# Optimization experiments

Measured on AMD Instinct MI355X. Metric: run time of the kernel, lower is better.

The kernel has to match this reference:

```python
import jax, jax.numpy as jnp
import numpy as np

B, S, D_IN, H, D_OUT = 32, 2048, 256, 512, 256


def setup_inputs() -> dict:
    key = jax.random.key(0)
    ks = jax.random.split(key, 12)
    sc = 0.02
    return {
        "x": jax.random.normal(ks[0], (B, S, D_IN), dtype=jnp.float32),
        # layer 0 (input_dim -> 4H), weights stored (in, out) so y = x @ W + b
        "Wx0": jax.random.normal(ks[1], (D_IN, 4 * H), dtype=jnp.float32) * sc,
        "bx0": jnp.zeros((4 * H,), dtype=jnp.float32),
        "Wh0": jax.random.normal(ks[2], (H, 4 * H), dtype=jnp.float32) * sc,
        "bh0": jnp.zeros((4 * H,), dtype=jnp.float32),
        # layer 1 (hidden -> 4H)
        "Wx1": jax.random.normal(ks[3], (H, 4 * H), dtype=jnp.float32) * sc,
        "bx1": jnp.zeros((4 * H,), dtype=jnp.float32),
        "Wh1": jax.random.normal(ks[4], (H, 4 * H), dtype=jnp.float32) * sc,
        "bh1": jnp.zeros((4 * H,), dtype=jnp.float32),
        # output projection
        "Wfc": jax.random.normal(ks[5], (H, D_OUT), dtype=jnp.float32) * sc,
        "bfc": jnp.zeros((D_OUT,), dtype=jnp.float32),
    }


def _cell(inp, h, c, Wx, bx, Wh, bh):
    # gates chunked in order f, i, g, o (matches torch chunk(4, dim=1))
    gates = inp @ Wx + bx + h @ Wh + bh  # [B, 4H]
    f, i, g, o = jnp.split(gates, 4, axis=1)
    c_new = jax.nn.sigmoid(f) * c + jax.nn.sigmoid(i) * jnp.tanh(g)
    h_new = jax.nn.sigmoid(o) * jnp.tanh(c_new)
    return h_new, c_new


def reference(x, Wx0, bx0, Wh0, bh0, Wx1, bx1, Wh1, bh1, Wfc, bfc):
    b = x.shape[0]
    hdim = Wh0.shape[0]

    def step(carry, xt):
        h0, c0, h1, c1 = carry
        h0, c0 = _cell(xt, h0, c0, Wx0, bx0, Wh0, bh0)
        h1, c1 = _cell(h0, h1, c1, Wx1, bx1, Wh1, bh1)
        return (h0, c0, h1, c1), h1

    init = tuple(jnp.zeros((b, hdim), x.dtype) for _ in range(4))
    x_tfirst = jnp.swapaxes(x, 0, 1)  # [S, B, D_in]
    _, outs = jax.lax.scan(step, init, x_tfirst)  # [S, B, H]
    outs = jnp.swapaxes(outs, 0, 1)  # [B, S, H]
    return outs @ Wfc + bfc  # [B, S, D_out]
```

## Files before the change

kernel.cpp:

```cpp
#include <hip/hip_runtime.h>
#include <math.h>

#define B_    32
#define S_    2048
#define DIN   256
#define H_    512
#define G_    2048
#define DOUT  256
#define T_    2048
#define NBLK  200

typedef __attribute__((ext_vector_type(8))) _Float16 f16x8;
typedef __attribute__((ext_vector_type(16))) float f32x16;
typedef __attribute__((ext_vector_type(2))) float f32x2;

#define MFMA(a,b,c) __builtin_amdgcn_mfma_f32_32x32x16_f16((a),(b),(c),0,0,0)

#define OB_SLOT      0u
#define OB_H0H       16384u
#define OB_H1H       147456u
#define OB_PART      278528u
#define OB_STATE_END 1327104u
#define OB_B0        1327104u
#define OB_B1        1335296u
#define OB_WF        1343488u
#define OB_W0        1605632u
#define OB_W1        4751360u
#define OB_END       8945664u
#define OB_XH        8945664u
#define OB_XEND      42500096u

#define LS_PT    49152
#define LS_CST   65536
#define LS_TOTAL 66560

__device__ __forceinline__ float sigf(float v) {
    return 1.0f / (1.0f + exp2f(-1.44269504f * v));
}
__device__ __forceinline__ float tanhfast(float v) {
    const float e = exp2f(2.88539008f * v);
    return 1.0f - 2.0f / (e + 1.0f);
}
__device__ __forceinline__ unsigned short h2u(_Float16 h) {
    union { _Float16 h; unsigned short u; } v; v.h = h; return v.u;
}

__device__ __forceinline__ f16x8 ld128_coh(const unsigned short* p) {
    f16x8 r;
    asm volatile("global_load_dwordx4 %0, %1, off sc0 sc1"
                 : "=v"(r) : "v"(p) : "memory");
    return r;
}
__device__ __forceinline__ f32x2 ld64f_coh(const float* p) {
    f32x2 r;
    asm volatile("global_load_dwordx2 %0, %1, off sc0 sc1"
                 : "=v"(r) : "v"(p) : "memory");
    return r;
}
__device__ __forceinline__ void st64f_coh(float* p, f32x2 v) {
    asm volatile("global_store_dwordx2 %0, %1, off sc0 sc1"
                 :: "v"(p), "v"(v) : "memory");
}
__device__ __forceinline__ int ld_slot(const int* slots, int i) {
    return __hip_atomic_load(&slots[i * 16], __ATOMIC_RELAXED, __HIP_MEMORY_SCOPE_AGENT);
}
__device__ __forceinline__ int packcol(int p) {
    return (((p >> 2) & 3) * H_) + ((p >> 4) << 2) + (p & 3);
}

__global__ __launch_bounds__(256) void repack_w(
    const float* __restrict__ s1, const float* __restrict__ s2,
    int k1, int K, int srcld, int dopack, unsigned short* __restrict__ dst)
{
    const int p  = blockIdx.x;
    const int kk = blockIdx.y * 256 + threadIdx.x;
    if (kk >= K) return;
    const int oc = dopack ? packcol(p) : p;
    const float w = (kk < k1) ? s1[(size_t)kk * srcld + oc]
                              : s2[(size_t)(kk - k1) * srcld + oc];
    dst[(size_t)p * K + kk] = h2u((_Float16)w);
}

__global__ __launch_bounds__(256) void repack_bias(
    const float* __restrict__ bx0, const float* __restrict__ bh0,
    const float* __restrict__ bx1, const float* __restrict__ bh1,
    char* __restrict__ wsb)
{
    const int q = blockIdx.x * 256 + threadIdx.x;
    if (q >= 2 * G_) return;
    const int p  = q & (G_ - 1);
    const int oc = packcol(p);
    float* dst = (float*)(wsb + (q < G_ ? OB_B0 : OB_B1));
    dst[p] = (q < G_) ? (bx0[oc] + bh0[oc]) : (bx1[oc] + bh1[oc]);
}

__global__ __launch_bounds__(256) void repack_x(const float* __restrict__ x, char* __restrict__ wsb)
{
    unsigned short* xh = (unsigned short*)(wsb + OB_XH);
    const size_t n = (size_t)B_ * S_ * DIN;
    for (size_t i = (size_t)blockIdx.x * 256 + threadIdx.x; i < n; i += (size_t)gridDim.x * 256)
        xh[i] = h2u((_Float16)x[i]);
}

__device__ __forceinline__ void phase_mm_l0(
    int k0, int colc, int halfl, int t, int xsplit,
    const float* __restrict__ x, const unsigned short* __restrict__ XH,
    const unsigned short* A1, const unsigned short* Wlds, f32x16& acc)
{
    f16x8 fh[6];
    #pragma unroll
    for (int s = 0; s < 6; ++s) {
        const int kf = k0 + s * 16;
        if (kf < 256) {
            const size_t o = ((size_t)colc * S_ + t) * DIN + kf + halfl * 8;
            if (xsplit) {
                fh[s] = *(const f16x8*)(XH + o);
            } else {
                const float* xp = x + o;
                #pragma unroll
                for (int j = 0; j < 8; ++j) fh[s][j] = (_Float16)xp[j];
            }
        } else {
            fh[s] = ld128_coh(A1 + colc * 512 + (kf - 256) + halfl * 8);
        }
    }
    asm volatile("s_waitcnt vmcnt(0)" ::: "memory");
    __builtin_amdgcn_sched_barrier(0);
    #pragma unroll
    for (int s = 0; s < 6; ++s) {
        const int k8a = ((k0 + s * 16) >> 3) + halfl;
        const f16x8 bw = *(const f16x8*)(Wlds + (k8a * 32 + colc) * 8);
        acc = MFMA(fh[s], bw, acc);
    }
}

__device__ __forceinline__ void phase_mm_single(
    int k0, int colc, int halfl,
    const unsigned short* A, const unsigned short* Wlds, f32x16& acc)
{
    f16x8 fh[4];
    #pragma unroll
    for (int s = 0; s < 4; ++s)
        fh[s] = ld128_coh(A + colc * 512 + (k0 + s * 16) + halfl * 8);
    asm volatile("s_waitcnt vmcnt(0)" ::: "memory");
    __builtin_amdgcn_sched_barrier(0);
    #pragma unroll
    for (int s = 0; s < 4; ++s) {
        const int k8a = ((k0 + s * 16) >> 3) + halfl;
        const f16x8 bw = *(const f16x8*)(Wlds + (k8a * 32 + colc) * 8);
        acc = MFMA(fh[s], bw, acc);
    }
}

__global__ __launch_bounds__(512, 2) void lstm_persist(
    const float* __restrict__ x, const float* __restrict__ bfc,
    float* __restrict__ out, char* __restrict__ wsb, int xsplit)
{
    extern __shared__ char smem[];
    unsigned short* Wlds = (unsigned short*)smem;
    float* Pt   = (float*)(smem + LS_PT);
    float* cstL = (float*)(smem + LS_CST);
    int* slots  = (int*)(wsb + OB_SLOT);

    const int blk = blockIdx.x, tid = threadIdx.x;
    const int wave = tid >> 6, lane = tid & 63;
    const int colc = lane & 31, halfl = lane >> 5;

    int role, bb;
    if (blk < 64)       { role = 0; bb = blk; }
    else if (blk < 128) { role = 1; bb = blk - 64; }
    else if (blk < 192) { role = 2; bb = blk - 128; }
    else                { role = 3; bb = blk - 192; }

    const int p0 = bb * 32;

    {
        const unsigned short* Wg;
        int wstride, rowoff, kcnt;
        if (role == 0)      { Wg = (const unsigned short*)(wsb + OB_W0); wstride = 768;  rowoff = 0;   kcnt = 768; }
        else if (role == 1) { Wg = (const unsigned short*)(wsb + OB_W1); wstride = 1024; rowoff = 0;   kcnt = 512; }
        else if (role == 2) { Wg = (const unsigned short*)(wsb + OB_W1); wstride = 1024; rowoff = 512; kcnt = 512; }
        else                { Wg = (const unsigned short*)(wsb + OB_WF); wstride = 512;  rowoff = 0;   kcnt = 512; }
        for (int idx = tid; idx < (kcnt >> 3) * 32; idx += 512) {
            const int k8 = idx >> 5, cl = idx & 31;
            *(f16x8*)(Wlds + idx * 8) =
                *(const f16x8*)(Wg + ((size_t)(p0 + cl) * wstride + rowoff + k8 * 8));
        }
    }
    for (int i = tid; i < 256; i += 512) cstL[i] = 0.f;
    __syncthreads();

    unsigned short* H0H = (unsigned short*)(wsb + OB_H0H);
    unsigned short* H1H = (unsigned short*)(wsb + OB_H1H);
    float* PART = (float*)(wsb + OB_PART);
    const unsigned short* XH = (const unsigned short*)(wsb + OB_XH);
    const float* Bp = (const float*)(wsb + (role == 2 ? OB_B1 : OB_B0));

    const int kcnt = (role == 0) ? 768 : 512;
    const int k0 = wave * (kcnt >> 3);
    int sA = 0, sB = 0, sC = 0;

    for (int t = 0; t < T_; ++t) {
        if (tid < 64) {
            if (role == 0) {
                const int tA = t, tB = t - 3;
                for (;;) {
                    bool ok = true;
                    if (sA < tA) sA = ld_slot(slots, lane);
                    ok = ok && (sA >= tA);
                    if (sB < tB) sB = ld_slot(slots, 64 + lane);
                    ok = ok && (sB >= tB);
                    if (__all(ok)) break;
                    __builtin_amdgcn_s_sleep(1);
                }
            } else if (role == 1) {
                const int tA = t + 1, tB = t - 3;
                for (;;) {
                    bool ok = true;
                    if (sA < tA) sA = ld_slot(slots, lane);
                    ok = ok && (sA >= tA);
                    if (lane == 0) {
                        if (sB < tB) sB = ld_slot(slots, 128 + bb);
                        ok = ok && (sB >= tB);
                    }
                    if (__all(ok)) break;
                    __builtin_amdgcn_s_sleep(1);
                }
            } else if (role == 2) {
                const int tA = t, tB = t + 1, tC = t - 3;
                for (;;) {
                    bool ok = true;
                    if (sA < tA) sA = ld_slot(slots, 128 + lane);
                    ok = ok && (sA >= tA);
                    if (lane == 0) {
                        if (sB < tB) sB = ld_slot(slots, 64 + bb);
                        ok = ok && (sB >= tB);
                    }
                    if (lane < 8) {
                        if (sC < tC) sC = ld_slot(slots, 192 + lane);
                        ok = ok && (sC >= tC);
                    }
                    if (__all(ok)) break;
                    __builtin_amdgcn_s_sleep(1);
                }
            } else {
                const int tA = t + 1;
                for (;;) {
                    if (sA < tA) sA = ld_slot(slots, 128 + lane);
                    if (__all(sA >= tA)) break;
                    __builtin_amdgcn_s_sleep(1);
                }
            }
        }
        __syncthreads();

        const int pw = t & 3, pr = (t + 3) & 3;

        f32x2 preg = {0.f, 0.f};
        if (role == 2)
            preg = ld64f_coh(PART + ((size_t)(pw * 64 + bb) << 10) + tid * 2);

        f32x16 acc;
        #pragma unroll
        for (int i = 0; i < 16; ++i) acc[i] = 0.f;

        if (role == 0)
            phase_mm_l0(k0, colc, halfl, t, xsplit, x, XH, H0H + pr * 16384, Wlds, acc);
        else if (role == 1)
            phase_mm_single(k0, colc, halfl, H0H + pw * 16384, Wlds, acc);
        else if (role == 2)
            phase_mm_single(k0, colc, halfl, H1H + pr * 16384, Wlds, acc);
        else
            phase_mm_single(k0, colc, halfl, H1H + pw * 16384, Wlds, acc);

        if (wave >= 4) {
            #pragma unroll
            for (int rg = 0; rg < 16; ++rg) {
                const int row = (rg & 3) + 8 * (rg >> 2) + 4 * halfl;
                Pt[(wave - 4) * 1024 + row * 32 + colc] = acc[rg];
            }
        }
        __syncthreads();
        if (wave < 4) {
            #pragma unroll
            for (int rg = 0; rg < 16; ++rg) {
                const int row = (rg & 3) + 8 * (rg >> 2) + 4 * halfl;
                Pt[wave * 1024 + row * 32 + colc] += acc[rg];
            }
        }
        __syncthreads();

        if (role == 1) {
            f32x2 pv;
            #pragma unroll
            for (int ii = 0; ii < 2; ++ii) {
                const int idx = tid * 2 + ii;
                pv[ii] = Pt[idx] + Pt[1024 + idx] + Pt[2048 + idx] + Pt[3072 + idx];
            }
            st64f_coh(PART + ((size_t)(pw * 64 + bb) << 10) + tid * 2, pv);
        } else if (role == 3) {
            #pragma unroll
            for (int ii = 0; ii < 2; ++ii) {
                const int idx = tid * 2 + ii;
                const int r = idx >> 5, c = idx & 31;
                const float v = Pt[idx] + Pt[1024 + idx] + Pt[2048 + idx] + Pt[3072 + idx]
                              + bfc[p0 + c];
                out[((size_t)r * S_ + t) * DOUT + p0 + c] = v;
            }
        } else {
            #pragma unroll
            for (int ii = 0; ii < 2; ++ii) {
                const int idx = tid * 2 + ii;
                float v = Pt[idx] + Pt[1024 + idx] + Pt[2048 + idx] + Pt[3072 + idx]
                        + Bp[p0 + (idx & 31)];
                if (role == 2) v += preg[ii];
                Pt[idx] = v;
            }
            __syncthreads();
            if (tid < 128) {
                const int r = tid >> 2, u2 = (tid & 3) * 2;
                const int cb = ((u2 >> 2) << 4) + (u2 & 3);
                unsigned short uh[2];
                #pragma unroll
                for (int uu = 0; uu < 2; ++uu) {
                    const float fg = Pt[r * 32 + cb + uu + 0];
                    const float ig = Pt[r * 32 + cb + uu + 4];
                    const float gg = Pt[r * 32 + cb + uu + 8];
                    const float og = Pt[r * 32 + cb + uu + 12];
                    const float cv = cstL[r * 8 + u2 + uu];
                    const float cn = sigf(fg) * cv + sigf(ig) * tanhfast(gg);
                    const float hn = sigf(og) * tanhfast(cn);
                    cstL[r * 8 + u2 + uu] = cn;
                    uh[uu] = h2u((_Float16)hn);
                }
                const unsigned wv = (unsigned)uh[0] | ((unsigned)uh[1] << 16);
                const int off = pw * 16384 + r * 512 + bb * 8 + u2;
                unsigned short* DH = (role == 0) ? H0H : H1H;
                __hip_atomic_store((unsigned*)(DH + off), wv,
                                   __ATOMIC_RELAXED, __HIP_MEMORY_SCOPE_AGENT);
            }
        }

        __syncthreads();
        if (tid == 0)
            __hip_atomic_store(&slots[blk * 16], t + 1,
                               __ATOMIC_RELAXED, __HIP_MEMORY_SCOPE_AGENT);
    }
}

extern "C" void kernel_launch(void* const* d_in, const int* in_sizes, int n_in,
                              void* d_out, int out_size, void* d_ws, size_t ws_size,
                              hipStream_t stream)
{
    const float* x   = (const float*)d_in[0];
    const float* Wx0 = (const float*)d_in[1];
    const float* bx0 = (const float*)d_in[2];
    const float* Wh0 = (const float*)d_in[3];
    const float* bh0 = (const float*)d_in[4];
    const float* Wx1 = (const float*)d_in[5];
    const float* bx1 = (const float*)d_in[6];
    const float* Wh1 = (const float*)d_in[7];
    const float* bh1 = (const float*)d_in[8];
    const float* Wfc = (const float*)d_in[9];
    const float* bfc = (const float*)d_in[10];
    float* out = (float*)d_out;
    char*  wsb = (char*)d_ws;

    const int xsplit = (ws_size >= OB_XEND) ? 1 : 0;

    hipMemsetAsync(d_ws, 0, OB_STATE_END, stream);

    repack_w<<<dim3(G_, 3), 256, 0, stream>>>(Wx0, Wh0, 256, 768, G_, 1,
        (unsigned short*)(wsb + OB_W0));
    repack_w<<<dim3(G_, 4), 256, 0, stream>>>(Wx1, Wh1, 512, 1024, G_, 1,
        (unsigned short*)(wsb + OB_W1));
    repack_w<<<dim3(DOUT, 2), 256, 0, stream>>>(Wfc, Wfc, 512, 512, DOUT, 0,
        (unsigned short*)(wsb + OB_WF));
    repack_bias<<<16, 256, 0, stream>>>(bx0, bh0, bx1, bh1, wsb);
    if (xsplit) repack_x<<<2048, 256, 0, stream>>>(x, wsb);

    hipFuncSetAttribute((const void*)lstm_persist,
                        hipFuncAttributeMaxDynamicSharedMemorySize, LS_TOTAL);
    lstm_persist<<<NBLK, 512, LS_TOTAL, stream>>>(x, bfc, out, wsb, xsplit);
}
```

Baseline: 9.212 ms.

## Store x and hidden states in MFMA-fragment order for contiguous wave loads

Rearranges the staged fp16 input copy and the H0/H1 hidden-state buffers so each 16-wide k-slice of the A operand for a 32x32x16 MFMA is stored as a contiguous 512-element block. Every lane then loads 16 contiguous bytes from one fully coalesced 1KB region, instead of 32 rows strided by 512 or 256 elements. The aim is fewer memory transactions and cache lines touched on the latency-critical recurrent loads each timestep. Producers now write h in the new interleaved layout, and the x repack kernel does a scattered gather to build it.

```diff
diff --git a/kernel.cpp b/kernel.cpp
--- a/kernel.cpp
+++ b/kernel.cpp
@@ -27,7 +27,7 @@
 #define OB_W0        1605632u
 #define OB_W1        4751360u
 #define OB_END       8945664u
-#define OB_XH        8945664u
+#define OB_XF        8945664u
 #define OB_XEND      42500096u
 
 #define LS_PT    49152
@@ -96,32 +96,39 @@
 
 __global__ __launch_bounds__(256) void repack_x(const float* __restrict__ x, char* __restrict__ wsb)
 {
-    unsigned short* xh = (unsigned short*)(wsb + OB_XH);
-    const size_t n = (size_t)B_ * S_ * DIN;
-    for (size_t i = (size_t)blockIdx.x * 256 + threadIdx.x; i < n; i += (size_t)gridDim.x * 256)
-        xh[i] = h2u((_Float16)x[i]);
+    unsigned short* xf = (unsigned short*)(wsb + OB_XF);
+    const size_t n = (size_t)S_ * 16 * 512;
+    for (size_t i = (size_t)blockIdx.x * 256 + threadIdx.x; i < n; i += (size_t)gridDim.x * 256) {
+        const int j  = (int)(i & 7);
+        const int l  = (int)((i >> 3) & 63);
+        const int kw = (int)((i >> 9) & 15);
+        const int t  = (int)(i >> 13);
+        const int r  = l & 31;
+        const int u  = kw * 16 + ((l >> 5) << 3) + j;
+        xf[i] = h2u((_Float16)x[((size_t)r * S_ + t) * DIN + u]);
+    }
 }
 
 __device__ __forceinline__ void phase_mm_l0(
-    int k0, int colc, int halfl, int t, int xsplit,
-    const float* __restrict__ x, const unsigned short* __restrict__ XH,
+    int k0, int lane, int t, int xsplit,
+    const float* __restrict__ x, const unsigned short* __restrict__ XF,
     const unsigned short* A1, const unsigned short* Wlds, f32x16& acc)
 {
+    const int colc = lane & 31, halfl = lane >> 5;
     f16x8 fh[6];
     #pragma unroll
     for (int s = 0; s < 6; ++s) {
         const int kf = k0 + s * 16;
         if (kf < 256) {
-            const size_t o = ((size_t)colc * S_ + t) * DIN + kf + halfl * 8;
             if (xsplit) {
-                fh[s] = *(const f16x8*)(XH + o);
+                fh[s] = *(const f16x8*)(XF + ((size_t)t * 16 + (kf >> 4)) * 512 + lane * 8);
             } else {
-                const float* xp = x + o;
+                const float* xp = x + ((size_t)colc * S_ + t) * DIN + kf + halfl * 8;
                 #pragma unroll
                 for (int j = 0; j < 8; ++j) fh[s][j] = (_Float16)xp[j];
             }
         } else {
-            fh[s] = ld128_coh(A1 + colc * 512 + (kf - 256) + halfl * 8);
+            fh[s] = ld128_coh(A1 + ((kf - 256) >> 4) * 512 + lane * 8);
         }
     }
     asm volatile("s_waitcnt vmcnt(0)" ::: "memory");
@@ -135,13 +142,14 @@
 }
 
 __device__ __forceinline__ void phase_mm_single(
-    int k0, int colc, int halfl,
+    int k0, int lane,
     const unsigned short* A, const unsigned short* Wlds, f32x16& acc)
 {
+    const int colc = lane & 31, halfl = lane >> 5;
     f16x8 fh[4];
     #pragma unroll
     for (int s = 0; s < 4; ++s)
-        fh[s] = ld128_coh(A + colc * 512 + (k0 + s * 16) + halfl * 8);
+        fh[s] = ld128_coh(A + ((k0 + s * 16) >> 4) * 512 + lane * 8);
     asm volatile("s_waitcnt vmcnt(0)" ::: "memory");
     __builtin_amdgcn_sched_barrier(0);
     #pragma unroll
@@ -176,12 +184,12 @@
 
     {
         const unsigned short* Wg;
-        int wstride, rowoff, kcnt;
-        if (role == 0)      { Wg = (const unsigned short*)(wsb + OB_W0); wstride = 768;  rowoff = 0;   kcnt = 768; }
-        else if (role == 1) { Wg = (const unsigned short*)(wsb + OB_W1); wstride = 1024; rowoff = 0;   kcnt = 512; }
-        else if (role == 2) { Wg = (const unsigned short*)(wsb + OB_W1); wstride = 1024; rowoff = 512; kcnt = 512; }
-        else                { Wg = (const unsigned short*)(wsb + OB_WF); wstride = 512;  rowoff = 0;   kcnt = 512; }
-        for (int idx = tid; idx < (kcnt >> 3) * 32; idx += 512) {
+        int wstride, rowoff, kcnt2;
+        if (role == 0)      { Wg = (const unsigned short*)(wsb + OB_W0); wstride = 768;  rowoff = 0;   kcnt2 = 768; }
+        else if (role == 1) { Wg = (const unsigned short*)(wsb + OB_W1); wstride = 1024; rowoff = 0;   kcnt2 = 512; }
+        else if (role == 2) { Wg = (const unsigned short*)(wsb + OB_W1); wstride = 1024; rowoff = 512; kcnt2 = 512; }
+        else                { Wg = (const unsigned short*)(wsb + OB_WF); wstride = 512;  rowoff = 0;   kcnt2 = 512; }
+        for (int idx = tid; idx < (kcnt2 >> 3) * 32; idx += 512) {
             const int k8 = idx >> 5, cl = idx & 31;
             *(f16x8*)(Wlds + idx * 8) =
                 *(const f16x8*)(Wg + ((size_t)(p0 + cl) * wstride + rowoff + k8 * 8));
@@ -193,7 +201,7 @@
     unsigned short* H0H = (unsigned short*)(wsb + OB_H0H);
     unsigned short* H1H = (unsigned short*)(wsb + OB_H1H);
     float* PART = (float*)(wsb + OB_PART);
-    const unsigned short* XH = (const unsigned short*)(wsb + OB_XH);
+    const unsigned short* XF = (const unsigned short*)(wsb + OB_XF);
     const float* Bp = (const float*)(wsb + (role == 2 ? OB_B1 : OB_B0));
 
     const int kcnt = (role == 0) ? 768 : 512;
@@ -265,13 +273,13 @@
         for (int i = 0; i < 16; ++i) acc[i] = 0.f;
 
         if (role == 0)
-            phase_mm_l0(k0, colc, halfl, t, xsplit, x, XH, H0H + pr * 16384, Wlds, acc);
+            phase_mm_l0(k0, lane, t, xsplit, x, XF, H0H + pr * 16384, Wlds, acc);
         else if (role == 1)
-            phase_mm_single(k0, colc, halfl, H0H + pw * 16384, Wlds, acc);
+            phase_mm_single(k0, lane, H0H + pw * 16384, Wlds, acc);
         else if (role == 2)
-            phase_mm_single(k0, colc, halfl, H1H + pr * 16384, Wlds, acc);
+            phase_mm_single(k0, lane, H1H + pr * 16384, Wlds, acc);
         else
-            phase_mm_single(k0, colc, halfl, H1H + pw * 16384, Wlds, acc);
+            phase_mm_single(k0, lane, H1H + pw * 16384, Wlds, acc);
 
         if (wave >= 4) {
             #pragma unroll
@@ -334,7 +342,8 @@
                     uh[uu] = h2u((_Float16)hn);
                 }
                 const unsigned wv = (unsigned)uh[0] | ((unsigned)uh[1] << 16);
-                const int off = pw * 16384 + r * 512 + bb * 8 + u2;
+                const int off = pw * 16384 + (bb >> 1) * 512
+                              + (r + ((bb & 1) << 5)) * 8 + u2;
                 unsigned short* DH = (role == 0) ? H0H : H1H;
                 __hip_atomic_store((unsigned*)(DH + off), wv,
                                    __ATOMIC_RELAXED, __HIP_MEMORY_SCOPE_AGENT);
```

Measured after the change: 9.323 ms. About the same (+1.2%).
